# Kernel optimization log

Measured on AMD Instinct MI355X. Metric: run time of the kernel, lower is better.

Reference implementation:

```python
import jax, jax.numpy as jnp
import numpy as np

NEG_INF = -1e30  # log-semiring zero
B, T, D, V, L = 16, 800, 512, 5000, 100


def setup_inputs() -> dict:
    key = jax.random.key(0)
    k1, k2, k3, k4, k5, k6 = jax.random.split(key, 6)
    hs_pad = jax.random.normal(k1, (B, T, D), dtype=jnp.float32)
    W = jax.random.normal(k2, (D, V), dtype=jnp.float32) / np.sqrt(D)
    b = jnp.zeros((V,), dtype=jnp.float32)
    hlens = jax.random.randint(k3, (B,), T // 2, T + 1, dtype=jnp.int32)
    labels = jax.random.randint(k4, (B, L), 1, V, dtype=jnp.int32)  # blank=0 excluded
    label_lens = jax.random.randint(k5, (B,), L // 2, L + 1, dtype=jnp.int32)
    return {"hs_pad": hs_pad, "W": W, "b": b, "hlens": hlens,
            "labels": labels, "label_lens": label_lens}


def _ctc_tot_scores(log_probs, hlens, labels, label_lens):
    # Standard CTC log-semiring forward DP (equivalent to k2 CTC-topology
    # intersect_dense + get_tot_scores). log_probs: [B,T,V], blank id = 0.
    Bb, Tt, Vv = log_probs.shape
    Ll = labels.shape[1]
    S = 2 * Ll + 1  # extended sequence: blank, l1, blank, l2, ..., blank
    ext = jnp.zeros((Bb, S), dtype=labels.dtype).at[:, 1::2].set(labels)
    # skip transition (s-2 -> s) allowed iff ext[s] != blank and ext[s] != ext[s-2]
    skip = jnp.concatenate(
        [jnp.zeros((Bb, 2), dtype=bool),
         (ext[:, 2:] != ext[:, :-2]) & (ext[:, 2:] != 0)], axis=1)
    # emissions along extended labels: lp_ext[b,t,s] = log_probs[b,t,ext[b,s]]
    lp_ext = jax.vmap(lambda lp, e: lp[:, e])(log_probs, ext)  # [B,T,S]
    alpha = jnp.full((Bb, S), NEG_INF, dtype=log_probs.dtype)
    alpha = alpha.at[:, 0].set(lp_ext[:, 0, 0])
    alpha = alpha.at[:, 1].set(lp_ext[:, 0, 1])

    def step(alpha, inp):
        t, lp_t = inp  # lp_t: [B,S]
        prev1 = jnp.pad(alpha[:, :-1], ((0, 0), (1, 0)), constant_values=NEG_INF)
        prev2 = jnp.pad(alpha[:, :-2], ((0, 0), (2, 0)), constant_values=NEG_INF)
        prev2 = jnp.where(skip, prev2, NEG_INF)
        a = jnp.logaddexp(jnp.logaddexp(alpha, prev1), prev2) + lp_t
        # freeze rows whose sequence has ended (t >= hlen)
        return jnp.where((t < hlens)[:, None], a, alpha), None

    ts = jnp.arange(1, Tt)
    alpha, _ = jax.lax.scan(step, alpha, (ts, jnp.swapaxes(lp_ext, 0, 1)[1:]))
    last = 2 * label_lens  # index of final blank per utterance
    a_last = jnp.take_along_axis(alpha, last[:, None], axis=1)[:, 0]
    a_prev = jnp.take_along_axis(alpha, (last - 1)[:, None], axis=1)[:, 0]
    return jnp.logaddexp(a_last, a_prev)  # [B] total log-likelihoods


def reference(hs_pad, W, b, hlens, labels, label_lens):
    # ctc_lo Linear (dropout_rate=0 -> identity) + log_softmax
    logits = jnp.einsum('btd,dv->btv', hs_pad, W) + b
    log_probs = jax.nn.log_softmax(logits, axis=-1)
    tot = _ctc_tot_scores(log_probs, hlens, labels, label_lens)
    # forward_scores = -tot_scores, reduce=True -> mean
    return jnp.mean(-tot)
```

## Files before the change

### kernel.cpp

```cpp
#include <hip/hip_runtime.h>

#define NEG_INF -1e30f

typedef __attribute__((ext_vector_type(8))) __bf16 bf16x8;
typedef __attribute__((ext_vector_type(4))) float f32x4;

constexpr int Bb = 16, T = 800, D = 512, V = 5000, L = 100;
constexpr int ROWS = Bb * T;
constexpr int S = 2 * L + 1;
constexpr int SP = 208;
constexpr int VP = 5120;
constexpr int NCB = VP / 128;
constexpr int NRB = ROWS / 128;
constexpr int NGB = Bb * 50;
constexpr int CONVB = ROWS * D / 1024;
constexpr int RSTRIDE = SP * 4;
constexpr int CH = 16;
constexpr int CHB = CH * RSTRIDE;

static __device__ __forceinline__ unsigned short f2bf(float x) {
  union { float f; unsigned u; } v; v.f = x;
  unsigned r = (v.u + 0x7FFFu + ((v.u >> 16) & 1u)) >> 16;
  return (unsigned short)r;
}

static __device__ __forceinline__ double dpp_shr1_zero_d(double x) {
  long long b = __double_as_longlong(x);
  int lo = (int)(b & 0xFFFFFFFFLL);
  int hi = (int)(b >> 32);
  int nlo = __builtin_amdgcn_update_dpp(0, lo, 0x138, 0xF, 0xF, false);
  int nhi = __builtin_amdgcn_update_dpp(0, hi, 0x138, 0xF, 0xF, false);
  return __longlong_as_double(((long long)(unsigned)nlo) | ((long long)nhi << 32));
}

static __device__ __forceinline__ float ex2(float x) { return __builtin_amdgcn_exp2f(x); }
static __device__ __forceinline__ float lg2(float x) { return __builtin_amdgcn_logf(x); }

static __device__ __forceinline__ float lg2d(double z) {
  long long b = __double_as_longlong(z);
  int e = (int)((b >> 52) & 0x7FF);
  if (e == 0) return -1.0e30f;
  unsigned mant = (unsigned)((b >> 29) & 0x7FFFFFu);
  float mf = __int_as_float(0x3F800000u | mant);
  return (float)(e - 1023) + lg2(mf);
}

__global__ __launch_bounds__(256) void k_prep(const float* __restrict__ hs,
                                              const float* __restrict__ W,
                                              unsigned short* __restrict__ A,
                                              unsigned short* __restrict__ Wt) {
  __shared__ float tile[64][65];
  int blk = blockIdx.x;
  if (blk < CONVB) {
    int i = blk * 256 + threadIdx.x;
    float4 f = ((const float4*)hs)[i];
    ushort4 o;
    o.x = f2bf(f.x); o.y = f2bf(f.y); o.z = f2bf(f.z); o.w = f2bf(f.w);
    ((ushort4*)A)[i] = o;
    return;
  }
  int g = blk - CONVB;
  int v0 = (g % (VP / 64)) * 64, k0 = (g / (VP / 64)) * 64;
  int tl = threadIdx.x & 63, th = threadIdx.x >> 6;
#pragma unroll
  for (int i = 0; i < 16; i++) {
    int k = k0 + th + i * 4;
    int v = v0 + tl;
    tile[th + i * 4][tl] = (v < V) ? W[(size_t)k * V + v] : 0.f;
  }
  __syncthreads();
#pragma unroll
  for (int i = 0; i < 16; i++) {
    int v = v0 + th + i * 4;
    int k = k0 + tl;
    Wt[(size_t)v * D + k] = f2bf(tile[tl][th + i * 4]);
  }
}

__global__ __launch_bounds__(256) void k_gather(const unsigned short* __restrict__ A,
                                                const unsigned short* __restrict__ Wt,
                                                const float* __restrict__ bias,
                                                const int* __restrict__ labels,
                                                float* __restrict__ glog) {
  int tid = threadIdx.x;
  int lane = tid & 63, w = tid >> 6;
  int q = lane >> 4, c = lane & 15;
  int b = blockIdx.x & 15, chk = blockIdx.x >> 4;
  int t0 = chk * 16;
  int bT = b * T, bL = b * L;
  int st0 = (w == 0) ? 0 : 4 + (w - 1) * 3;
  int nst = (w == 0) ? 4 : 3;

  int evs[4]; float bvs[4];
#pragma unroll
  for (int j = 0; j < 4; j++) {
    int st = st0 + (j < nst ? j : nst - 1);
    int s = st * 16 + c;
    evs[j] = (s < S && (s & 1)) ? labels[bL + (s >> 1)] : 0;
    bvs[j] = bias[evs[j]];
  }
  const unsigned short* Arow = A + (size_t)(bT + t0 + c) * D;
  f32x4 acc[4];
#pragma unroll
  for (int j = 0; j < 4; j++) acc[j] = (f32x4){0.f, 0.f, 0.f, 0.f};
  for (int kk = 0; kk < D; kk += 32) {
    bf16x8 aa = *(const bf16x8*)(Arow + kk + q * 8);
#pragma unroll
    for (int j = 0; j < 4; j++) {
      bf16x8 bb = *(const bf16x8*)(Wt + (size_t)evs[j] * D + kk + q * 8);
      acc[j] = __builtin_amdgcn_mfma_f32_16x16x32_bf16(aa, bb, acc[j], 0, 0, 0);
    }
  }
#pragma unroll
  for (int j = 0; j < 4; j++) {
    if (j >= nst) break;
    int st = st0 + j;
#pragma unroll
    for (int r = 0; r < 4; r++)
      glog[(size_t)(bT + t0 + q * 4 + r) * SP + st * 16 + c] = acc[j][r] + bvs[j];
  }
}

__global__ __launch_bounds__(256) void k_fused(const unsigned short* __restrict__ A,
                                               const unsigned short* __restrict__ Wt,
                                               const float* __restrict__ bias,
                                               const float* __restrict__ glog,
                                               const int* __restrict__ labels,
                                               const int* __restrict__ hlens,
                                               const int* __restrict__ llens,
                                               float* __restrict__ partM,
                                               float* __restrict__ partS,
                                               float* __restrict__ rawtot) {
  __shared__ __attribute__((aligned(16))) char smem[34816];

  int blk = blockIdx.x;
  if (blk < Bb) {
    if (threadIdx.x >= 64) return;
    __builtin_amdgcn_s_setprio(1);
    int b = blk, l = threadIdx.x;
    int col4 = ((4 * l < SP) ? 4 * l : SP - 4) * 4;
    const char* gvb = (const char*)glog + (size_t)b * T * RSTRIDE;
    int hl = hlens[b];
    int nch = (hl - 1 + CH - 1) / CH;
    const size_t gmax = (size_t)T * RSTRIDE - 16;

    auto stage = [&](int cc, int dst) {
      size_t sb = (size_t)(1 + cc * CH) * RSTRIDE;
#pragma unroll
      for (int pg = 0; pg < 13; pg++) {
        size_t ob = sb + (size_t)pg * 1024 + (size_t)l * 16;
        if (ob > gmax) ob = gmax;
        __builtin_amdgcn_global_load_lds(
            (const __attribute__((address_space(1))) void*)(gvb + ob),
            (__attribute__((address_space(3))) void*)(smem + dst * CHB + pg * 1024),
            16, 0, 0);
      }
    };

    int i0 = (2 * l < L) ? 2 * l : L - 1;
    int i1 = (2 * l + 1 < L) ? 2 * l + 1 : L - 1;
    int im = (l >= 1) ? 2 * l - 1 : 0; im = im < L ? im : L - 1;
    int lab0 = labels[b * L + i0];
    int lab1 = labels[b * L + i1];
    int labm = labels[b * L + im];
    bool sk1 = (l >= 1) && (lab0 != 0) && (lab0 != labm);
    bool sk3 = (lab1 != 0) && (lab1 != lab0);

    constexpr float LOG2E = 1.44269504f;
    f32x4 g0 = *(const f32x4*)(gvb + col4);
    double z0 = (l == 0) ? 1.0 : 0.0;
    double z1 = (l == 0) ? (double)ex2((g0.y - g0.x) * LOG2E) : 0.0;
    double z2 = 0.0, z3 = 0.0;
    double Csum = (double)g0.x;
    int Kc = 0;

    stage(0, 0);
    stage(1, 1);

#define DP_STEPZ(G) {                                                  \
    double e1 = (double)ex2(((G).y - (G).x) * LOG2E);                  \
    double e3 = (double)ex2(((G).w - (G).x) * LOG2E);                  \
    Csum += (double)(G).x;                                             \
    double p3 = dpp_shr1_zero_d(z3);                                   \
    double nz0 = z0 + p3;                                              \
    double nz1 = (z1 + z0 + (sk1 ? p3 : 0.0)) * e1;                    \
    double nz2 = z2 + z1;                                              \
    double nz3 = (z3 + z2 + (sk3 ? z1 : 0.0)) * e3;                    \
    z0 = nz0; z1 = nz1; z2 = nz2; z3 = nz3; }

    for (int c = 0; c < nch; ++c) {
      int cur = c & 1;
      if (c + 2 < nch) { asm volatile("s_waitcnt vmcnt(13)" ::: "memory"); }
      else             { asm volatile("s_waitcnt vmcnt(0)"  ::: "memory"); }
      __builtin_amdgcn_sched_barrier(0);
      const char* bufc = smem + cur * CHB + col4;
      int steps = hl - 1 - c * CH; if (steps > CH) steps = CH;
      if (steps == CH) {
        f32x4 G[8];
#pragma unroll
        for (int j = 0; j < 8; j++) G[j] = *(const f32x4*)(bufc + j * RSTRIDE);
#pragma unroll
        for (int j = 0; j < 8; j++) DP_STEPZ(G[j])
#pragma unroll
        for (int j = 0; j < 8; j++) G[j] = *(const f32x4*)(bufc + (8 + j) * RSTRIDE);
#pragma unroll
        for (int j = 0; j < 8; j++) DP_STEPZ(G[j])
        long long bz0 = __double_as_longlong(z0), bz1 = __double_as_longlong(z1);
        long long bz2 = __double_as_longlong(z2), bz3 = __double_as_longlong(z3);
        int e0 = (int)((bz0 >> 52) & 0x7FF), e1i = (int)((bz1 >> 52) & 0x7FF);
        int e2i = (int)((bz2 >> 52) & 0x7FF), e3i = (int)((bz3 >> 52) & 0x7FF);
        int em = e0 > e1i ? e0 : e1i;
        em = em > e2i ? em : e2i;
        em = em > e3i ? em : e3i;
#pragma unroll
        for (int o = 1; o < 64; o <<= 1) { int q2 = __shfl_xor(em, o); em = em > q2 ? em : q2; }
        if (em > 0 && em < 2046) {
          double sc = __longlong_as_double((long long)(2046 - em) << 52);
          z0 *= sc; z1 *= sc; z2 *= sc; z3 *= sc;
          Kc += em - 1023;
        }
      } else {
        for (int j = 0; j < steps; j++) {
          f32x4 G = *(const f32x4*)(bufc + j * RSTRIDE);
          DP_STEPZ(G)
        }
      }
      if (c + 2 < nch) {
        asm volatile("s_waitcnt lgkmcnt(0)" ::: "memory");
        stage(c + 2, cur);
      }
    }
#undef DP_STEPZ

    int ll = llens[b];
    int s1i = 2 * ll, s2i = 2 * ll - 1;
    int c1 = s1i & 3, c2 = s2i & 3;
    float lz0 = lg2d(z0), lz1 = lg2d(z1), lz2 = lg2d(z2), lz3 = lg2d(z3);
    float cand1 = c1 == 0 ? lz0 : c1 == 1 ? lz1 : c1 == 2 ? lz2 : lz3;
    float cand2 = c2 == 0 ? lz0 : c2 == 1 ? lz1 : c2 == 2 ? lz2 : lz3;
    float v1 = __shfl(cand1, s1i >> 2);
    float v2 = __shfl(cand2, s2i >> 2);
    if (l == 0) {
      float m = fmaxf(v1, v2);
      float d = m + lg2(ex2(v1 - m) + ex2(v2 - m));
      rawtot[b] = (float)(Csum + 0.6931471805599453 * ((double)Kc + (double)d));
    }
    return;
  }

  unsigned short* As = (unsigned short*)smem;
  unsigned short* Bs = (unsigned short*)(smem + 16384);
  float (*redM)[128] = (float (*)[128])(smem + 32768);
  float (*redS)[128] = (float (*)[128])(smem + 33792);

  int gblk = blk - Bb;
  int cb = gblk % NCB, rb = gblk / NCB;
  int tid = threadIdx.x;
  int lane = tid & 63, w = tid >> 6;
  int q = lane >> 4, c = lane & 15;
  int mh = w & 1, nh = w >> 1;
  int row0 = rb * 128, n0 = cb * 128;
  int lr = lane >> 3, lc = lane & 7;
  int oc = (lc ^ lr) * 8;

  f32x4 acc[4][4];
#pragma unroll
  for (int mt = 0; mt < 4; mt++)
#pragma unroll
    for (int nt = 0; nt < 4; nt++) acc[mt][nt] = (f32x4){0.f, 0.f, 0.f, 0.f};

  for (int kk = 0; kk < D; kk += 64) {
#pragma unroll
    for (int j = 0; j < 4; j++) {
      int i = w * 4 + j;
      const unsigned short* ga = A + (size_t)(row0 + i * 8 + lr) * D + kk + oc;
      __builtin_amdgcn_global_load_lds(
          (const __attribute__((address_space(1))) void*)ga,
          (__attribute__((address_space(3))) void*)(As + i * 512), 16, 0, 0);
      const unsigned short* gb = Wt + (size_t)(n0 + i * 8 + lr) * D + kk + oc;
      __builtin_amdgcn_global_load_lds(
          (const __attribute__((address_space(1))) void*)gb,
          (__attribute__((address_space(3))) void*)(Bs + i * 512), 16, 0, 0);
    }
    __syncthreads();
#pragma unroll
    for (int kq = 0; kq < 2; kq++) {
      int o = ((kq * 4 + q) ^ (c & 7)) * 8;
      bf16x8 af[4], bfr[4];
#pragma unroll
      for (int mt = 0; mt < 4; mt++)
        af[mt] = *(const bf16x8*)(As + (mh * 64 + mt * 16 + c) * 64 + o);
#pragma unroll
      for (int nt = 0; nt < 4; nt++)
        bfr[nt] = *(const bf16x8*)(Bs + (nh * 64 + nt * 16 + c) * 64 + o);
#pragma unroll
      for (int mt = 0; mt < 4; mt++)
#pragma unroll
        for (int nt = 0; nt < 4; nt++)
          acc[mt][nt] = __builtin_amdgcn_mfma_f32_16x16x32_bf16(af[mt], bfr[nt], acc[mt][nt], 0, 0, 0);
    }
    __syncthreads();
  }

  int vcb[4]; float bv[4];
#pragma unroll
  for (int nt = 0; nt < 4; nt++) {
    vcb[nt] = n0 + nh * 64 + nt * 16 + c;
    bv[nt] = (vcb[nt] < V) ? bias[vcb[nt]] : 0.f;
  }
#pragma unroll
  for (int mt = 0; mt < 4; mt++) {
#pragma unroll
    for (int r = 0; r < 4; r++) {
      float x[4]; float m = NEG_INF;
#pragma unroll
      for (int nt = 0; nt < 4; nt++) {
        x[nt] = (vcb[nt] < V) ? (acc[mt][nt][r] + bv[nt]) : NEG_INF;
        m = fmaxf(m, x[nt]);
      }
#pragma unroll
      for (int o = 1; o < 16; o <<= 1) m = fmaxf(m, __shfl_xor(m, o));
      float s = 0.f;
#pragma unroll
      for (int nt = 0; nt < 4; nt++) s += __expf(x[nt] - m);
#pragma unroll
      for (int o = 1; o < 16; o <<= 1) s += __shfl_xor(s, o);
      if (c == 0) {
        int rloc = mh * 64 + mt * 16 + q * 4 + r;
        redM[nh][rloc] = m;
        redS[nh][rloc] = s;
      }
    }
  }
  __syncthreads();
  if (tid < 128) {
    float m0 = redM[0][tid], m1 = redM[1][tid];
    float mm = fmaxf(m0, m1);
    float ss = redS[0][tid] * __expf(m0 - mm) + redS[1][tid] * __expf(m1 - mm);
    partM[(size_t)cb * ROWS + row0 + tid] = mm;
    partS[(size_t)cb * ROWS + row0 + tid] = ss;
  }
}

__global__ __launch_bounds__(256) void k_lse(const float* __restrict__ pM,
                                             const float* __restrict__ pS,
                                             float* __restrict__ lse) {
  int row = blockIdx.x * 256 + threadIdx.x;
  float m = pM[row], s = pS[row];
  for (int cb = 1; cb < NCB; cb++) {
    float M2 = pM[(size_t)cb * ROWS + row], S2 = pS[(size_t)cb * ROWS + row];
    float mn = fmaxf(m, M2);
    s = s * __expf(m - mn) + S2 * __expf(M2 - mn);
    m = mn;
  }
  lse[row] = m + __logf(s);
}

__global__ __launch_bounds__(1024) void k_final(const float* __restrict__ lse,
                                                const float* __restrict__ rawtot,
                                                const int* __restrict__ hlens,
                                                float* __restrict__ out) {
  __shared__ float acc[Bb];
  int w = threadIdx.x >> 6, l = threadIdx.x & 63;
  int hl = hlens[w];
  float s = 0.f;
  for (int t = l; t < hl; t += 64) s += lse[w * T + t];
#pragma unroll
  for (int o = 1; o < 64; o <<= 1) s += __shfl_xor(s, o);
  if (l == 0) acc[w] = rawtot[w] - s;
  __syncthreads();
  if (threadIdx.x == 0) {
    float m = 0.f;
    for (int i = 0; i < Bb; i++) m += acc[i];
    out[0] = -m / (float)Bb;
  }
}

extern "C" void kernel_launch(void* const* d_in, const int* in_sizes, int n_in,
                              void* d_out, int out_size, void* d_ws, size_t ws_size,
                              hipStream_t stream) {
  const float* hs    = (const float*)d_in[0];
  const float* W     = (const float*)d_in[1];
  const float* bias  = (const float*)d_in[2];
  const int* hlens   = (const int*)d_in[3];
  const int* labels  = (const int*)d_in[4];
  const int* llens   = (const int*)d_in[5];
  float* out = (float*)d_out;

  char* ws = (char*)d_ws;
  unsigned short* A    = (unsigned short*)(ws);
  unsigned short* Wt   = (unsigned short*)(ws + 13107200);
  float*          partM= (float*)(ws + 18350080);
  float*          partS= (float*)(ws + 20398080);
  float*          lse  = (float*)(ws + 22446080);
  float*          glog = (float*)(ws + 22497280);
  float*          rawtot=(float*)(ws + 33146880);

  k_prep<<<CONVB + (VP / 64) * (D / 64), 256, 0, stream>>>(hs, W, A, Wt);
  k_gather<<<NGB, 256, 0, stream>>>(A, Wt, bias, labels, glog);
  k_fused<<<Bb + NCB * NRB, 256, 0, stream>>>(A, Wt, bias, glog, labels, hlens, llens,
                                              partM, partS, rawtot);
  k_lse<<<ROWS / 256, 256, 0, stream>>>(partM, partS, lse);
  k_final<<<1, 1024, 0, stream>>>(lse, rawtot, hlens, out);

  (void)in_sizes; (void)n_in; (void)out_size; (void)ws_size;
}
```

Before: 267.2 us.

## Split CTC recursion into concurrent forward and backward halves meeting at midpoint

The serial CTC alpha recursion per utterance is split across two wavefronts: one runs the forward DP over the first half of frames and the other runs a backward (beta) DP from the final states over the second half. The two results are combined at the midpoint with a log-sum-exp over all states. The aim is to roughly halve the serial dependency chain that bounds the DP blocks. The change also shrinks staging chunks to 8 frames and computes the exponentials in float. In exchange it adds a block barrier, an extra reduction and new backward-recursion code, and the combination step is a new source of numerical differences.

```diff
diff --git a/kernel.cpp b/kernel.cpp
--- a/kernel.cpp
+++ b/kernel.cpp
@@ -15,8 +15,8 @@
 constexpr int NGB = Bb * 50;
 constexpr int CONVB = ROWS * D / 1024;
 constexpr int RSTRIDE = SP * 4;
-constexpr int CH = 16;
-constexpr int CHB = CH * RSTRIDE;
+constexpr int CH = 8;
+constexpr int CHB = 7168;
 
 static __device__ __forceinline__ unsigned short f2bf(float x) {
   union { float f; unsigned u; } v; v.f = x;
@@ -30,6 +30,14 @@
   int hi = (int)(b >> 32);
   int nlo = __builtin_amdgcn_update_dpp(0, lo, 0x138, 0xF, 0xF, false);
   int nhi = __builtin_amdgcn_update_dpp(0, hi, 0x138, 0xF, 0xF, false);
+  return __longlong_as_double(((long long)(unsigned)nlo) | ((long long)nhi << 32));
+}
+static __device__ __forceinline__ double dpp_shl1_zero_d(double x) {
+  long long b = __double_as_longlong(x);
+  int lo = (int)(b & 0xFFFFFFFFLL);
+  int hi = (int)(b >> 32);
+  int nlo = __builtin_amdgcn_update_dpp(0, lo, 0x130, 0xF, 0xF, false);
+  int nhi = __builtin_amdgcn_update_dpp(0, hi, 0x130, 0xF, 0xF, false);
   return __longlong_as_double(((long long)(unsigned)nlo) | ((long long)nhi << 32));
 }
 
@@ -121,6 +129,22 @@
   }
 }
 
+#define RENORM4(A0, A1, A2, A3, KC) {                                           \
+    long long ba0 = __double_as_longlong(A0), ba1 = __double_as_longlong(A1);   \
+    long long ba2 = __double_as_longlong(A2), ba3 = __double_as_longlong(A3);   \
+    int ee0 = (int)((ba0 >> 52) & 0x7FF), ee1 = (int)((ba1 >> 52) & 0x7FF);     \
+    int ee2 = (int)((ba2 >> 52) & 0x7FF), ee3 = (int)((ba3 >> 52) & 0x7FF);     \
+    int em = ee0 > ee1 ? ee0 : ee1;                                             \
+    em = em > ee2 ? em : ee2;                                                   \
+    em = em > ee3 ? em : ee3;                                                   \
+    _Pragma("unroll")                                                           \
+    for (int o = 1; o < 64; o <<= 1) { int q2 = __shfl_xor(em, o); em = em > q2 ? em : q2; } \
+    if (em > 0 && em < 2046) {                                                  \
+      double sc = __longlong_as_double((long long)(2046 - em) << 52);           \
+      A0 *= sc; A1 *= sc; A2 *= sc; A3 *= sc;                                   \
+      KC += em - 1023;                                                          \
+    } }
+
 __global__ __launch_bounds__(256) void k_fused(const unsigned short* __restrict__ A,
                                                const unsigned short* __restrict__ Wt,
                                                const float* __restrict__ bias,
@@ -135,27 +159,16 @@
 
   int blk = blockIdx.x;
   if (blk < Bb) {
-    if (threadIdx.x >= 64) return;
-    __builtin_amdgcn_s_setprio(1);
-    int b = blk, l = threadIdx.x;
+    int tid = threadIdx.x;
+    int w = tid >> 6, l = tid & 63;
+    if (w >= 2) { __syncthreads(); return; }
+
+    int b = blk;
     int col4 = ((4 * l < SP) ? 4 * l : SP - 4) * 4;
     const char* gvb = (const char*)glog + (size_t)b * T * RSTRIDE;
     int hl = hlens[b];
-    int nch = (hl - 1 + CH - 1) / CH;
+    int mfw = (hl - 1) >> 1;
     const size_t gmax = (size_t)T * RSTRIDE - 16;
-
-    auto stage = [&](int cc, int dst) {
-      size_t sb = (size_t)(1 + cc * CH) * RSTRIDE;
-#pragma unroll
-      for (int pg = 0; pg < 13; pg++) {
-        size_t ob = sb + (size_t)pg * 1024 + (size_t)l * 16;
-        if (ob > gmax) ob = gmax;
-        __builtin_amdgcn_global_load_lds(
-            (const __attribute__((address_space(1))) void*)(gvb + ob),
-            (__attribute__((address_space(3))) void*)(smem + dst * CHB + pg * 1024),
-            16, 0, 0);
-      }
-    };
 
     int i0 = (2 * l < L) ? 2 * l : L - 1;
     int i1 = (2 * l + 1 < L) ? 2 * l + 1 : L - 1;
@@ -167,83 +180,174 @@
     bool sk3 = (lab1 != 0) && (lab1 != lab0);
 
     constexpr float LOG2E = 1.44269504f;
-    f32x4 g0 = *(const f32x4*)(gvb + col4);
-    double z0 = (l == 0) ? 1.0 : 0.0;
-    double z1 = (l == 0) ? (double)ex2((g0.y - g0.x) * LOG2E) : 0.0;
-    double z2 = 0.0, z3 = 0.0;
-    double Csum = (double)g0.x;
-    int Kc = 0;
-
-    stage(0, 0);
-    stage(1, 1);
-
-#define DP_STEPZ(G) {                                                  \
-    double e1 = (double)ex2(((G).y - (G).x) * LOG2E);                  \
-    double e3 = (double)ex2(((G).w - (G).x) * LOG2E);                  \
+    float* laf = (float*)(smem + 28672);
+    float* lbf = (float*)(smem + 29504);
+
+    if (w == 0) {
+      f32x4 g0 = *(const f32x4*)(gvb + col4);
+      double z0 = (l == 0) ? 1.0 : 0.0;
+      double z1 = (l == 0) ? (double)ex2((g0.y - g0.x) * LOG2E) : 0.0;
+      double z2 = 0.0, z3 = 0.0;
+      double Csum = (double)g0.x;
+      int Kc = 0;
+
+      auto stageF = [&](int cc, int dst) {
+        size_t sb = (size_t)(1 + cc * CH) * RSTRIDE;
+#pragma unroll
+        for (int pg = 0; pg < 7; pg++) {
+          size_t ob = sb + (size_t)pg * 1024 + (size_t)l * 16;
+          if (ob > gmax) ob = gmax;
+          __builtin_amdgcn_global_load_lds(
+              (const __attribute__((address_space(1))) void*)(gvb + ob),
+              (__attribute__((address_space(3))) void*)(smem + dst * CHB + pg * 1024),
+              16, 0, 0);
+        }
+      };
+
+#define FW_STEPZ(G) {                                                  \
+    float e1f = ex2(((G).y - (G).x) * LOG2E);                          \
+    float e3f = ex2(((G).w - (G).x) * LOG2E);                          \
     Csum += (double)(G).x;                                             \
     double p3 = dpp_shr1_zero_d(z3);                                   \
     double nz0 = z0 + p3;                                              \
-    double nz1 = (z1 + z0 + (sk1 ? p3 : 0.0)) * e1;                    \
+    double nz1 = (z1 + z0 + (sk1 ? p3 : 0.0)) * (double)e1f;           \
     double nz2 = z2 + z1;                                              \
-    double nz3 = (z3 + z2 + (sk3 ? z1 : 0.0)) * e3;                    \
+    double nz3 = (z3 + z2 + (sk3 ? z1 : 0.0)) * (double)e3f;           \
     z0 = nz0; z1 = nz1; z2 = nz2; z3 = nz3; }
 
-    for (int c = 0; c < nch; ++c) {
-      int cur = c & 1;
-      if (c + 2 < nch) { asm volatile("s_waitcnt vmcnt(13)" ::: "memory"); }
-      else             { asm volatile("s_waitcnt vmcnt(0)"  ::: "memory"); }
-      __builtin_amdgcn_sched_barrier(0);
-      const char* bufc = smem + cur * CHB + col4;
-      int steps = hl - 1 - c * CH; if (steps > CH) steps = CH;
-      if (steps == CH) {
-        f32x4 G[8];
-#pragma unroll
-        for (int j = 0; j < 8; j++) G[j] = *(const f32x4*)(bufc + j * RSTRIDE);
-#pragma unroll
-        for (int j = 0; j < 8; j++) DP_STEPZ(G[j])
-#pragma unroll
-        for (int j = 0; j < 8; j++) G[j] = *(const f32x4*)(bufc + (8 + j) * RSTRIDE);
-#pragma unroll
-        for (int j = 0; j < 8; j++) DP_STEPZ(G[j])
-        long long bz0 = __double_as_longlong(z0), bz1 = __double_as_longlong(z1);
-        long long bz2 = __double_as_longlong(z2), bz3 = __double_as_longlong(z3);
-        int e0 = (int)((bz0 >> 52) & 0x7FF), e1i = (int)((bz1 >> 52) & 0x7FF);
-        int e2i = (int)((bz2 >> 52) & 0x7FF), e3i = (int)((bz3 >> 52) & 0x7FF);
-        int em = e0 > e1i ? e0 : e1i;
-        em = em > e2i ? em : e2i;
-        em = em > e3i ? em : e3i;
-#pragma unroll
-        for (int o = 1; o < 64; o <<= 1) { int q2 = __shfl_xor(em, o); em = em > q2 ? em : q2; }
-        if (em > 0 && em < 2046) {
-          double sc = __longlong_as_double((long long)(2046 - em) << 52);
-          z0 *= sc; z1 *= sc; z2 *= sc; z3 *= sc;
-          Kc += em - 1023;
+      int nchF = (mfw + CH - 1) / CH;
+      stageF(0, 0);
+      stageF(1, 1);
+      for (int c = 0; c < nchF; ++c) {
+        int cur = c & 1;
+        if (c + 2 < nchF) { asm volatile("s_waitcnt vmcnt(7)" ::: "memory"); }
+        else             { asm volatile("s_waitcnt vmcnt(0)" ::: "memory"); }
+        __builtin_amdgcn_sched_barrier(0);
+        const char* bufc = smem + cur * CHB + col4;
+        int steps = mfw - c * CH; if (steps > CH) steps = CH;
+        if (steps == CH) {
+          f32x4 G[8];
+#pragma unroll
+          for (int j = 0; j < 8; j++) G[j] = *(const f32x4*)(bufc + j * RSTRIDE);
+#pragma unroll
+          for (int j = 0; j < 8; j++) FW_STEPZ(G[j])
+          RENORM4(z0, z1, z2, z3, Kc)
+        } else {
+          for (int j = 0; j < steps; j++) {
+            f32x4 G = *(const f32x4*)(bufc + j * RSTRIDE);
+            FW_STEPZ(G)
+          }
         }
-      } else {
-        for (int j = 0; j < steps; j++) {
-          f32x4 G = *(const f32x4*)(bufc + j * RSTRIDE);
-          DP_STEPZ(G)
+        if (c + 2 < nchF) {
+          asm volatile("s_waitcnt lgkmcnt(0)" ::: "memory");
+          stageF(c + 2, cur);
         }
       }
-      if (c + 2 < nch) {
-        asm volatile("s_waitcnt lgkmcnt(0)" ::: "memory");
-        stage(c + 2, cur);
+#undef FW_STEPZ
+      if (l < 52) {
+        float base = (float)(Csum * 1.4426950408889634 + (double)Kc);
+        laf[4 * l + 0] = base + lg2d(z0);
+        laf[4 * l + 1] = base + lg2d(z1);
+        laf[4 * l + 2] = base + lg2d(z2);
+        laf[4 * l + 3] = base + lg2d(z3);
+      }
+    } else {
+      int ll = llens[b];
+      int sA = 2 * ll, sB = sA - 1;
+      int s0i = 4 * l;
+      double b0 = (s0i == sA || s0i == sB) ? 1.0 : 0.0;
+      double b1 = (s0i + 1 == sA || s0i + 1 == sB) ? 1.0 : 0.0;
+      double b2 = (s0i + 2 == sA || s0i + 2 == sB) ? 1.0 : 0.0;
+      double b3 = (s0i + 3 == sA || s0i + 3 == sB) ? 1.0 : 0.0;
+      double Csum = 0.0;
+      int Kc = 0;
+      int sk1i = sk1 ? 1 : 0;
+      bool sk1n = __shfl_down(sk1i, 1) != 0;
+
+      auto stageB = [&](int cc, int dst) {
+        int rlo = hl - 1 - cc * CH - 7;
+        size_t sb = (size_t)rlo * RSTRIDE;
+#pragma unroll
+        for (int pg = 0; pg < 7; pg++) {
+          size_t ob = sb + (size_t)pg * 1024 + (size_t)l * 16;
+          if (ob > gmax) ob = gmax;
+          __builtin_amdgcn_global_load_lds(
+              (const __attribute__((address_space(1))) void*)(gvb + ob),
+              (__attribute__((address_space(3))) void*)(smem + dst * CHB + pg * 1024),
+              16, 0, 0);
+        }
+      };
+
+#define BW_STEPZ(G) {                                                  \
+    float e1f = ex2(((G).y - (G).x) * LOG2E);                          \
+    float e3f = ex2(((G).w - (G).x) * LOG2E);                          \
+    Csum += (double)(G).x;                                             \
+    double f1 = b1 * (double)e1f;                                      \
+    double f3 = b3 * (double)e3f;                                      \
+    double q4 = dpp_shl1_zero_d(b0);                                   \
+    double q5 = dpp_shl1_zero_d(f1);                                   \
+    double nb0 = b0 + f1;                                              \
+    double nb1 = f1 + b2 + (sk3 ? f3 : 0.0);                           \
+    double nb2 = b2 + f3;                                              \
+    double nb3 = f3 + q4 + (sk1n ? q5 : 0.0);                          \
+    b0 = nb0; b1 = nb1; b2 = nb2; b3 = nb3; }
+
+      int bsteps = (hl - 1) - mfw;
+      int nchB = (bsteps + CH - 1) / CH;
+      stageB(0, 2);
+      stageB(1, 3);
+      for (int c = 0; c < nchB; ++c) {
+        int cur = c & 1;
+        if (c + 2 < nchB) { asm volatile("s_waitcnt vmcnt(7)" ::: "memory"); }
+        else             { asm volatile("s_waitcnt vmcnt(0)" ::: "memory"); }
+        __builtin_amdgcn_sched_barrier(0);
+        const char* bufc = smem + (2 + cur) * CHB + col4;
+        int hi = hl - 1 - c * CH;
+        int steps = hi - mfw; if (steps > CH) steps = CH;
+        if (steps == CH) {
+          f32x4 G[8];
+#pragma unroll
+          for (int j = 0; j < 8; j++) G[j] = *(const f32x4*)(bufc + (7 - j) * RSTRIDE);
+#pragma unroll
+          for (int j = 0; j < 8; j++) BW_STEPZ(G[j])
+          RENORM4(b0, b1, b2, b3, Kc)
+        } else {
+          for (int j = 0; j < steps; j++) {
+            f32x4 G = *(const f32x4*)(bufc + (7 - j) * RSTRIDE);
+            BW_STEPZ(G)
+          }
+        }
+        if (c + 2 < nchB) {
+          asm volatile("s_waitcnt lgkmcnt(0)" ::: "memory");
+          stageB(c + 2, 2 + cur);
+        }
+      }
+#undef BW_STEPZ
+      if (l < 52) {
+        float base = (float)(Csum * 1.4426950408889634 + (double)Kc);
+        lbf[4 * l + 0] = base + lg2d(b0);
+        lbf[4 * l + 1] = base + lg2d(b1);
+        lbf[4 * l + 2] = base + lg2d(b2);
+        lbf[4 * l + 3] = base + lg2d(b3);
       }
     }
-#undef DP_STEPZ
-
-    int ll = llens[b];
-    int s1i = 2 * ll, s2i = 2 * ll - 1;
-    int c1 = s1i & 3, c2 = s2i & 3;
-    float lz0 = lg2d(z0), lz1 = lg2d(z1), lz2 = lg2d(z2), lz3 = lg2d(z3);
-    float cand1 = c1 == 0 ? lz0 : c1 == 1 ? lz1 : c1 == 2 ? lz2 : lz3;
-    float cand2 = c2 == 0 ? lz0 : c2 == 1 ? lz1 : c2 == 2 ? lz2 : lz3;
-    float v1 = __shfl(cand1, s1i >> 2);
-    float v2 = __shfl(cand2, s2i >> 2);
-    if (l == 0) {
-      float m = fmaxf(v1, v2);
-      float d = m + lg2(ex2(v1 - m) + ex2(v2 - m));
-      rawtot[b] = (float)(Csum + 0.6931471805599453 * ((double)Kc + (double)d));
+
+    __syncthreads();
+    if (w == 0) {
+      float v[4];
+#pragma unroll
+      for (int r = 0; r < 4; r++) {
+        int s = 4 * l + r;
+        v[r] = (l < 52 && s < S) ? (laf[s] + lbf[s]) : -1.0e30f;
+      }
+      float mx = fmaxf(fmaxf(v[0], v[1]), fmaxf(v[2], v[3]));
+#pragma unroll
+      for (int o = 1; o < 64; o <<= 1) mx = fmaxf(mx, __shfl_xor(mx, o));
+      float ssum = ex2(v[0] - mx) + ex2(v[1] - mx) + ex2(v[2] - mx) + ex2(v[3] - mx);
+#pragma unroll
+      for (int o = 1; o < 64; o <<= 1) ssum += __shfl_xor(ssum, o);
+      if (l == 0)
+        rawtot[b] = 0.6931471805599453f * (mx + lg2(ssum));
     }
     return;
   }
```

Measured after the change: 262.6 us. About the same (-1.7%).
